# Performance work log

Measured on AMD Instinct MI355X. Metric: run time of the kernel, lower is better.

Reference implementation:

```python
import jax, jax.numpy as jnp
import numpy as np

EPSILON_BASE = 0.1
N_ITERS = 10


def setup_inputs() -> dict:
    key = jax.random.key(0)
    k1, k2 = jax.random.split(key)
    N, D = 8192, 512
    embeddings = jax.random.normal(k1, (N, D), dtype=jnp.float32)
    target_noise = jax.random.normal(k2, (N, D), dtype=jnp.float32)
    return {"embeddings": embeddings, "target_noise": target_noise}


def _l2_normalize(x, axis=1, eps=1e-12):
    # matches torch.nn.functional.normalize (divide by max(norm, eps))
    norm = jnp.sqrt(jnp.sum(x * x, axis=axis, keepdims=True))
    return x / jnp.maximum(norm, eps)


def _sinkhorn(x, y):
    n, d = x.shape
    # normalize_embeddings=True path
    x = _l2_normalize(x, axis=1)
    y = _l2_normalize(y, axis=1)
    epsilon = EPSILON_BASE * 2.0
    # squared euclidean cost: C[i,j] = ||x_i - y_j||^2  (cdist p=2, squared)
    sq_x = jnp.sum(x * x, axis=1, keepdims=True)          # (n,1)
    sq_y = jnp.sum(y * y, axis=1, keepdims=True)          # (n,1)
    C = jnp.maximum(sq_x + sq_y.T - 2.0 * (x @ y.T), 0.0)  # (n,n)
    log_K = -C / epsilon

    def body(carry, _):
        log_u, log_v = carry
        log_u = -jax.nn.logsumexp(log_K + log_v[None, :], axis=1)
        log_v = -jax.nn.logsumexp(log_K.T + log_u[None, :], axis=1)
        return (log_u, log_v), None

    init = (jnp.zeros(n, dtype=x.dtype), jnp.zeros(n, dtype=y.dtype))
    (log_u, log_v), _ = jax.lax.scan(body, init, None, length=N_ITERS)

    log_P = log_u[:, None] + log_K + log_v[None, :]
    P = jnp.clip(jnp.exp(log_P), 0.0, 1.0)
    distance = jnp.sum(P * C) / n

    # nan/inf fallback: 1 - mean cosine similarity (x, y already unit norm)
    fallback = 1.0 - jnp.mean(jnp.sum(x * y, axis=1))
    bad = jnp.isnan(distance) | jnp.isinf(distance)
    return jnp.where(bad, fallback, distance)


def reference(embeddings, target_noise):
    if embeddings.ndim == 3:
        embeddings = embeddings.reshape(-1, embeddings.shape[-1])
        target_noise = target_noise.reshape(-1, target_noise.shape[-1])
    return _sinkhorn(embeddings, target_noise)
```

## Files before the change

### kernel.cpp

```cpp
#include <hip/hip_runtime.h>
#include <hip/hip_bf16.h>
#include <hip/hip_fp16.h>
#include <stdint.h>

#define NROW 8192
#define DIM  512
#define LN2   0.6931471805599453f
#define TEN_LOG2E 14.426950408889634f

typedef __attribute__((ext_vector_type(8))) short short8;
typedef __attribute__((ext_vector_type(4))) float f32x4;
typedef __attribute__((ext_vector_type(2))) float f32x2;

__device__ __forceinline__ float block_sum256(float v) {
  #pragma unroll
  for (int off = 32; off > 0; off >>= 1) v += __shfl_down(v, off, 64);
  __shared__ float sb[4];
  const int w = threadIdx.x >> 6;
  if ((threadIdx.x & 63) == 0) sb[w] = v;
  __syncthreads();
  return sb[0] + sb[1] + sb[2] + sb[3];
}

__global__ __launch_bounds__(256) void init_kernel(float* __restrict__ colrcp,
                                                   float* __restrict__ diagacc,
                                                   float* __restrict__ distacc) {
  const int g = blockIdx.x * 256 + threadIdx.x;
  colrcp[g] = 1.0f;
  if (g == 0) { diagacc[0] = 0.f; distacc[0] = 0.f; }
}

__global__ __launch_bounds__(256) void normalize_kernel(
    const float* __restrict__ X, const float* __restrict__ Y,
    __hip_bfloat16* __restrict__ Xn, __hip_bfloat16* __restrict__ Yn,
    float* __restrict__ diagacc) {
  const int wave = threadIdx.x >> 6, lane = threadIdx.x & 63;
  float dsum = 0.f;
  #pragma unroll
  for (int rr = 0; rr < 4; rr++) {
    const int row = blockIdx.x * 16 + wave * 4 + rr;
    const float4* xr = (const float4*)(X + (size_t)row * DIM);
    const float4* yr = (const float4*)(Y + (size_t)row * DIM);
    float4 x0 = xr[lane], x1 = xr[lane + 64];
    float4 y0 = yr[lane], y1 = yr[lane + 64];
    float sx = x0.x*x0.x + x0.y*x0.y + x0.z*x0.z + x0.w*x0.w
             + x1.x*x1.x + x1.y*x1.y + x1.z*x1.z + x1.w*x1.w;
    float sy = y0.x*y0.x + y0.y*y0.y + y0.z*y0.z + y0.w*y0.w
             + y1.x*y1.x + y1.y*y1.y + y1.z*y1.z + y1.w*y1.w;
    float sxy = x0.x*y0.x + x0.y*y0.y + x0.z*y0.z + x0.w*y0.w
              + x1.x*y1.x + x1.y*y1.y + x1.z*y1.z + x1.w*y1.w;
    #pragma unroll
    for (int off = 1; off < 64; off <<= 1) {
      sx  += __shfl_xor(sx, off, 64);
      sy  += __shfl_xor(sy, off, 64);
      sxy += __shfl_xor(sxy, off, 64);
    }
    const float rx = 1.0f / fmaxf(sqrtf(sx), 1e-12f);
    const float ry = 1.0f / fmaxf(sqrtf(sy), 1e-12f);
    if (lane == 0) dsum += sxy * rx * ry;
    ushort4 px, py;
    { __hip_bfloat16 b;
      b = __float2bfloat16(x0.x*rx); px.x = *(unsigned short*)&b;
      b = __float2bfloat16(x0.y*rx); px.y = *(unsigned short*)&b;
      b = __float2bfloat16(x0.z*rx); px.z = *(unsigned short*)&b;
      b = __float2bfloat16(x0.w*rx); px.w = *(unsigned short*)&b;
      b = __float2bfloat16(y0.x*ry); py.x = *(unsigned short*)&b;
      b = __float2bfloat16(y0.y*ry); py.y = *(unsigned short*)&b;
      b = __float2bfloat16(y0.z*ry); py.z = *(unsigned short*)&b;
      b = __float2bfloat16(y0.w*ry); py.w = *(unsigned short*)&b;
    }
    ((ushort4*)(Xn + (size_t)row * DIM))[lane] = px;
    ((ushort4*)(Yn + (size_t)row * DIM))[lane] = py;
    { __hip_bfloat16 b;
      b = __float2bfloat16(x1.x*rx); px.x = *(unsigned short*)&b;
      b = __float2bfloat16(x1.y*rx); px.y = *(unsigned short*)&b;
      b = __float2bfloat16(x1.z*rx); px.z = *(unsigned short*)&b;
      b = __float2bfloat16(x1.w*rx); px.w = *(unsigned short*)&b;
      b = __float2bfloat16(y1.x*ry); py.x = *(unsigned short*)&b;
      b = __float2bfloat16(y1.y*ry); py.y = *(unsigned short*)&b;
      b = __float2bfloat16(y1.z*ry); py.z = *(unsigned short*)&b;
      b = __float2bfloat16(y1.w*ry); py.w = *(unsigned short*)&b;
    }
    ((ushort4*)(Xn + (size_t)row * DIM))[lane + 64] = px;
    ((ushort4*)(Yn + (size_t)row * DIM))[lane + 64] = py;
  }
  if (lane == 0) atomicAdd(diagacc, dsum);
}

__global__ __launch_bounds__(256) void gemm_kernel(
    const __hip_bfloat16* __restrict__ A, const __hip_bfloat16* __restrict__ B,
    uint8_t* __restrict__ K, uint8_t* __restrict__ KT) {
  __shared__ int4 smem4[1024];
  short* As = (short*)smem4;
  short* Bs = As + 128 * 32;
  const int m0 = blockIdx.y * 128;
  const int n0 = blockIdx.x * 128;
  const int t = threadIdx.x;
  const int wave = t >> 6, lane = t & 63;
  const int wm = (wave & 1) * 64, wn = (wave >> 1) * 64;
  const int fr = lane & 15;
  const int fq = lane >> 4;

  f32x4 acc[4][4];
  #pragma unroll
  for (int i = 0; i < 4; i++)
    #pragma unroll
    for (int j = 0; j < 4; j++) acc[i][j] = (f32x4)0.f;

  const int L0 = t, L1 = t + 256;
  const int ar0 = L0 >> 2, ac0 = L0 & 3;
  const int ar1 = L1 >> 2, ac1 = L1 & 3;
  const int4* Ag = (const int4*)A;
  const int4* Bg = (const int4*)B;

  for (int kt = 0; kt < 16; ++kt) {
    const int kb = kt * 4;
    int4 a0 = Ag[(size_t)(m0 + ar0) * 64 + kb + ac0];
    int4 a1 = Ag[(size_t)(m0 + ar1) * 64 + kb + ac1];
    int4 b0 = Bg[(size_t)(n0 + ar0) * 64 + kb + ac0];
    int4 b1 = Bg[(size_t)(n0 + ar1) * 64 + kb + ac1];
    __syncthreads();
    ((int4*)As)[L0] = a0;
    ((int4*)As)[L1] = a1;
    ((int4*)Bs)[L0] = b0;
    ((int4*)Bs)[L1] = b1;
    __syncthreads();
    short8 af[4], bfr[4];
    #pragma unroll
    for (int i = 0; i < 4; i++) {
      af[i]  = *(const short8*)&As[(wm + i * 16 + fr) * 32 + fq * 8];
      bfr[i] = *(const short8*)&Bs[(wn + i * 16 + fr) * 32 + fq * 8];
    }
    #pragma unroll
    for (int i = 0; i < 4; i++)
      #pragma unroll
      for (int j = 0; j < 4; j++)
        acc[i][j] = __builtin_amdgcn_mfma_f32_16x16x32_bf16(af[i], bfr[j], acc[i][j], 0, 0, 0);
  }
  __syncthreads();
  uint8_t* tile = (uint8_t*)smem4;
  #pragma unroll
  for (int i = 0; i < 4; i++) {
    #pragma unroll
    for (int j = 0; j < 4; j++) {
      const int R  = wm + i * 16 + fq * 4;
      const int Cc = wn + j * 16 + fr;
      float v0 = exp2f(fminf(acc[i][j][0], 1.0f) * TEN_LOG2E);
      float v1 = exp2f(fminf(acc[i][j][1], 1.0f) * TEN_LOG2E);
      float v2 = exp2f(fminf(acc[i][j][2], 1.0f) * TEN_LOG2E);
      float v3 = exp2f(fminf(acc[i][j][3], 1.0f) * TEN_LOG2E);
      int pk = 0;
      pk = __builtin_amdgcn_cvt_pk_fp8_f32(v0, v1, pk, false);
      pk = __builtin_amdgcn_cvt_pk_fp8_f32(v2, v3, pk, true);
      const int a = Cc * 128 + R;
      *(int*)(tile + (a ^ (((a >> 7) & 7) << 4))) = pk;
      uint8_t* kp = K + (size_t)(m0 + R) * NROW + n0 + Cc;
      kp[0]            = (uint8_t)(pk & 0xff);
      kp[NROW]         = (uint8_t)((pk >> 8) & 0xff);
      kp[2 * NROW]     = (uint8_t)((pk >> 16) & 0xff);
      kp[3 * NROW]     = (uint8_t)((pk >> 24) & 0xff);
    }
  }
  __syncthreads();
  {
    const int r = t >> 1, h = (t & 1) * 64;
    uint8_t* gp = KT + (size_t)(n0 + r) * NROW + m0 + h;
    #pragma unroll
    for (int q = 0; q < 4; q++) {
      const int a = r * 128 + h + q * 16;
      *(int4*)(gp + q * 16) = *(const int4*)(tile + (a ^ (((a >> 7) & 7) << 4)));
    }
  }
}

__global__ __launch_bounds__(256) void pass_kernel(
    const uint8_t* __restrict__ M, const float* __restrict__ w,
    float* __restrict__ out) {
  __shared__ float4 wl[2048];
  const int t = threadIdx.x;
  #pragma unroll
  for (int c = 0; c < 8; c++) {
    const int j = c * 256 + t;
    wl[j ^ ((j >> 3) & 3)] = ((const float4*)w)[j];
  }
  __syncthreads();
  const int wave = t >> 6, lane = t & 63;
  const int row = blockIdx.x * 4 + wave;
  const int xh = (lane >> 1) & 3;
  const int4* Mr = (const int4*)(M + (size_t)row * NROW);
  int4 k[8];
  #pragma unroll
  for (int c = 0; c < 8; c++) k[c] = Mr[c * 64 + lane];
  float acc0 = 0.f, acc1 = 0.f;
  #pragma unroll
  for (int c = 0; c < 8; c++) {
    const int b4 = (c * 64 + lane) * 4;
    const int* kd = (const int*)&k[c];
    #pragma unroll
    for (int q = 0; q < 4; q++) {
      float4 ww = wl[b4 + (q ^ xh)];
      f32x2 lo = __builtin_amdgcn_cvt_pk_f32_fp8(kd[q], false);
      f32x2 hi = __builtin_amdgcn_cvt_pk_f32_fp8(kd[q], true);
      acc0 += lo.x * ww.x + lo.y * ww.y;
      acc1 += hi.x * ww.z + hi.y * ww.w;
    }
  }
  float acc = acc0 + acc1;
  #pragma unroll
  for (int off = 32; off > 0; off >>= 1) acc += __shfl_down(acc, off, 64);
  if (lane == 0) out[row] = 1.0f / acc;
}

__global__ __launch_bounds__(256) void dist_kernel(
    const uint8_t* __restrict__ K, const float* __restrict__ v,
    const float* __restrict__ u, float* __restrict__ distacc) {
  __shared__ float4 wl[2048];
  const int t = threadIdx.x;
  #pragma unroll
  for (int c = 0; c < 8; c++) {
    const int j = c * 256 + t;
    wl[j ^ ((j >> 3) & 3)] = ((const float4*)v)[j];
  }
  __syncthreads();
  const int wave = t >> 6, lane = t & 63;
  const int row = blockIdx.x * 4 + wave;
  const int xh = (lane >> 1) & 3;
  const float ui = u[row];
  const int4* Kr = (const int4*)(K + (size_t)row * NROW);
  float acc = 0.f;
  #pragma unroll 2
  for (int c = 0; c < 8; c++) {
    int4 kq = Kr[c * 64 + lane];
    const int b4 = (c * 64 + lane) * 4;
    const int* kd = (const int*)&kq;
    #pragma unroll
    for (int q = 0; q < 4; q++) {
      float4 ww = wl[b4 + (q ^ xh)];
      f32x2 lo = __builtin_amdgcn_cvt_pk_f32_fp8(kd[q], false);
      f32x2 hi = __builtin_amdgcn_cvt_pk_f32_fp8(kd[q], true);
      float kv[4] = {lo.x, lo.y, hi.x, hi.y};
      float wv[4] = {ww.x, ww.y, ww.z, ww.w};
      #pragma unroll
      for (int e = 0; e < 4; e++) {
        float p = fminf(ui * kv[e] * wv[e], 1.f);
        float cterm = 2.f - 0.2f * LN2 * __log2f(fmaxf(kv[e], 1e-6f));
        acc += p * cterm;
      }
    }
  }
  float tot = block_sum256(acc);
  if (t == 0) atomicAdd(distacc, tot);
}

__global__ void final_kernel(const float* __restrict__ distacc,
                             const float* __restrict__ diagacc,
                             float* __restrict__ out) {
  if (threadIdx.x == 0 && blockIdx.x == 0) {
    float d = distacc[0] * (1.0f / (float)NROW);
    float fb = 1.0f - diagacc[0] * (1.0f / (float)NROW);
    float v = (isnan(d) || isinf(d)) ? fb : d;
    __hip_bfloat16 b = __float2bfloat16(v);
    unsigned short h = *(unsigned short*)&b;
    ((unsigned int*)out)[0] = ((unsigned int)h << 16) | (unsigned int)h;
  }
}

extern "C" void kernel_launch(void* const* d_in, const int* in_sizes, int n_in,
                              void* d_out, int out_size, void* d_ws, size_t ws_size,
                              hipStream_t stream) {
  (void)in_sizes; (void)n_in; (void)out_size; (void)ws_size;
  const float* X = (const float*)d_in[0];
  const float* Y = (const float*)d_in[1];
  float* out = (float*)d_out;

  char* ws = (char*)d_ws;
  size_t off = 0;
  uint8_t* K  = (uint8_t*)(ws + off); off += (size_t)NROW * NROW;
  uint8_t* KT = (uint8_t*)(ws + off); off += (size_t)NROW * NROW;
  __hip_bfloat16* Xn = (__hip_bfloat16*)(ws + off); off += (size_t)NROW * DIM * 2;
  __hip_bfloat16* Yn = (__hip_bfloat16*)(ws + off); off += (size_t)NROW * DIM * 2;
  float* rowrcp  = (float*)(ws + off); off += NROW * 4;
  float* colrcp  = (float*)(ws + off); off += NROW * 4;
  float* diagacc = (float*)(ws + off); off += 256;
  float* distacc = (float*)(ws + off); off += 256;

  init_kernel<<<32, 256, 0, stream>>>(colrcp, diagacc, distacc);
  normalize_kernel<<<512, 256, 0, stream>>>(X, Y, Xn, Yn, diagacc);
  gemm_kernel<<<dim3(64, 64), 256, 0, stream>>>(Xn, Yn, K, KT);
  for (int it = 0; it < 10; ++it) {
    pass_kernel<<<2048, 256, 0, stream>>>(K,  colrcp, rowrcp);
    pass_kernel<<<2048, 256, 0, stream>>>(KT, rowrcp, colrcp);
  }
  dist_kernel<<<2048, 256, 0, stream>>>(K, colrcp, rowrcp, distacc);
  final_kernel<<<1, 64, 0, stream>>>(distacc, diagacc, out);
}
```

Before: 489.2 us.

## Fuse final column pass with distance and process four rows per wave

Each wave in the pass kernel now handles four rows, double-buffering the next row's fp8 loads in registers. The weight vector is staged into LDS once per 16 rows instead of once per 4. The last column-scaling pass is merged into the distance kernel, which reads KT and computes v_j in registers before accumulating P*C, removing one full 64MB matrix sweep. The cost is fewer blocks (512) and higher register use, which may lower occupancy.

Result: no change. 493.2 us (+0.8%).

```diff
diff --git a/kernel.cpp b/kernel.cpp
--- a/kernel.cpp
+++ b/kernel.cpp
@@ -178,77 +178,115 @@
     float* __restrict__ out) {
   __shared__ float4 wl[2048];
   const int t = threadIdx.x;
+  const int wave = t >> 6, lane = t & 63;
+  const int xh = (lane >> 1) & 3;
+  const int row0 = blockIdx.x * 16 + wave * 4;
+  int4 ka[8], kb[8];
+  const int4* Mr0 = (const int4*)(M + (size_t)row0 * NROW);
+  #pragma unroll
+  for (int c = 0; c < 8; c++) ka[c] = Mr0[c * 64 + lane];
   #pragma unroll
   for (int c = 0; c < 8; c++) {
     const int j = c * 256 + t;
     wl[j ^ ((j >> 3) & 3)] = ((const float4*)w)[j];
   }
   __syncthreads();
-  const int wave = t >> 6, lane = t & 63;
-  const int row = blockIdx.x * 4 + wave;
-  const int xh = (lane >> 1) & 3;
-  const int4* Mr = (const int4*)(M + (size_t)row * NROW);
-  int4 k[8];
-  #pragma unroll
-  for (int c = 0; c < 8; c++) k[c] = Mr[c * 64 + lane];
-  float acc0 = 0.f, acc1 = 0.f;
-  #pragma unroll
-  for (int c = 0; c < 8; c++) {
-    const int b4 = (c * 64 + lane) * 4;
-    const int* kd = (const int*)&k[c];
-    #pragma unroll
-    for (int q = 0; q < 4; q++) {
-      float4 ww = wl[b4 + (q ^ xh)];
-      f32x2 lo = __builtin_amdgcn_cvt_pk_f32_fp8(kd[q], false);
-      f32x2 hi = __builtin_amdgcn_cvt_pk_f32_fp8(kd[q], true);
-      acc0 += lo.x * ww.x + lo.y * ww.y;
-      acc1 += hi.x * ww.z + hi.y * ww.w;
-    }
-  }
-  float acc = acc0 + acc1;
-  #pragma unroll
-  for (int off = 32; off > 0; off >>= 1) acc += __shfl_down(acc, off, 64);
-  if (lane == 0) out[row] = 1.0f / acc;
-}
-
-__global__ __launch_bounds__(256) void dist_kernel(
-    const uint8_t* __restrict__ K, const float* __restrict__ v,
-    const float* __restrict__ u, float* __restrict__ distacc) {
+  #pragma unroll
+  for (int r = 0; r < 4; r++) {
+    if (r < 3) {
+      const int4* Mn = (const int4*)(M + (size_t)(row0 + r + 1) * NROW);
+      #pragma unroll
+      for (int c = 0; c < 8; c++) { if (r & 1) ka[c] = Mn[c * 64 + lane]; else kb[c] = Mn[c * 64 + lane]; }
+    }
+    float acc0 = 0.f, acc1 = 0.f;
+    #pragma unroll
+    for (int c = 0; c < 8; c++) {
+      const int b4 = (c * 64 + lane) * 4;
+      const int4 kc = (r & 1) ? kb[c] : ka[c];
+      const int* kd = (const int*)&kc;
+      #pragma unroll
+      for (int q = 0; q < 4; q++) {
+        float4 ww = wl[b4 + (q ^ xh)];
+        f32x2 lo = __builtin_amdgcn_cvt_pk_f32_fp8(kd[q], false);
+        f32x2 hi = __builtin_amdgcn_cvt_pk_f32_fp8(kd[q], true);
+        acc0 += lo.x * ww.x + lo.y * ww.y;
+        acc1 += hi.x * ww.z + hi.y * ww.w;
+      }
+    }
+    float acc = acc0 + acc1;
+    #pragma unroll
+    for (int off = 32; off > 0; off >>= 1) acc += __shfl_down(acc, off, 64);
+    if (lane == 0) out[row0 + r] = 1.0f / acc;
+  }
+}
+
+__global__ __launch_bounds__(256) void pass_dist_kernel(
+    const uint8_t* __restrict__ KT, const float* __restrict__ u,
+    float* __restrict__ distacc) {
   __shared__ float4 wl[2048];
   const int t = threadIdx.x;
+  const int wave = t >> 6, lane = t & 63;
+  const int xh = (lane >> 1) & 3;
+  const int row0 = blockIdx.x * 16 + wave * 4;
+  int4 ka[8], kb[8];
+  const int4* Mr0 = (const int4*)(KT + (size_t)row0 * NROW);
+  #pragma unroll
+  for (int c = 0; c < 8; c++) ka[c] = Mr0[c * 64 + lane];
   #pragma unroll
   for (int c = 0; c < 8; c++) {
     const int j = c * 256 + t;
-    wl[j ^ ((j >> 3) & 3)] = ((const float4*)v)[j];
-  }
-  __syncthreads();
-  const int wave = t >> 6, lane = t & 63;
-  const int row = blockIdx.x * 4 + wave;
-  const int xh = (lane >> 1) & 3;
-  const float ui = u[row];
-  const int4* Kr = (const int4*)(K + (size_t)row * NROW);
-  float acc = 0.f;
-  #pragma unroll 2
-  for (int c = 0; c < 8; c++) {
-    int4 kq = Kr[c * 64 + lane];
-    const int b4 = (c * 64 + lane) * 4;
-    const int* kd = (const int*)&kq;
-    #pragma unroll
-    for (int q = 0; q < 4; q++) {
-      float4 ww = wl[b4 + (q ^ xh)];
-      f32x2 lo = __builtin_amdgcn_cvt_pk_f32_fp8(kd[q], false);
-      f32x2 hi = __builtin_amdgcn_cvt_pk_f32_fp8(kd[q], true);
-      float kv[4] = {lo.x, lo.y, hi.x, hi.y};
-      float wv[4] = {ww.x, ww.y, ww.z, ww.w};
-      #pragma unroll
-      for (int e = 0; e < 4; e++) {
-        float p = fminf(ui * kv[e] * wv[e], 1.f);
-        float cterm = 2.f - 0.2f * LN2 * __log2f(fmaxf(kv[e], 1e-6f));
-        acc += p * cterm;
+    wl[j ^ ((j >> 3) & 3)] = ((const float4*)u)[j];
+  }
+  __syncthreads();
+  float accd = 0.f;
+  #pragma unroll
+  for (int r = 0; r < 4; r++) {
+    if (r < 3) {
+      const int4* Mn = (const int4*)(KT + (size_t)(row0 + r + 1) * NROW);
+      #pragma unroll
+      for (int c = 0; c < 8; c++) { if (r & 1) ka[c] = Mn[c * 64 + lane]; else kb[c] = Mn[c * 64 + lane]; }
+    }
+    float acc0 = 0.f, acc1 = 0.f;
+    #pragma unroll
+    for (int c = 0; c < 8; c++) {
+      const int b4 = (c * 64 + lane) * 4;
+      const int4 kc = (r & 1) ? kb[c] : ka[c];
+      const int* kd = (const int*)&kc;
+      #pragma unroll
+      for (int q = 0; q < 4; q++) {
+        float4 ww = wl[b4 + (q ^ xh)];
+        f32x2 lo = __builtin_amdgcn_cvt_pk_f32_fp8(kd[q], false);
+        f32x2 hi = __builtin_amdgcn_cvt_pk_f32_fp8(kd[q], true);
+        acc0 += lo.x * ww.x + lo.y * ww.y;
+        acc1 += hi.x * ww.z + hi.y * ww.w;
       }
     }
-  }
-  float tot = block_sum256(acc);
+    float s = acc0 + acc1;
+    #pragma unroll
+    for (int off = 1; off < 64; off <<= 1) s += __shfl_xor(s, off, 64);
+    const float vj = 1.0f / s;
+    #pragma unroll
+    for (int c = 0; c < 8; c++) {
+      const int b4 = (c * 64 + lane) * 4;
+      const int4 kc = (r & 1) ? kb[c] : ka[c];
+      const int* kd = (const int*)&kc;
+      #pragma unroll
+      for (int q = 0; q < 4; q++) {
+        float4 ww = wl[b4 + (q ^ xh)];
+        f32x2 lo = __builtin_amdgcn_cvt_pk_f32_fp8(kd[q], false);
+        f32x2 hi = __builtin_amdgcn_cvt_pk_f32_fp8(kd[q], true);
+        float kv[4] = {lo.x, lo.y, hi.x, hi.y};
+        float uv[4] = {ww.x, ww.y, ww.z, ww.w};
+        #pragma unroll
+        for (int e = 0; e < 4; e++) {
+          float p = fminf(uv[e] * kv[e] * vj, 1.f);
+          float cterm = 2.f - 0.2f * LN2 * __log2f(fmaxf(kv[e], 1e-6f));
+          accd += p * cterm;
+        }
+      }
+    }
+  }
+  float tot = block_sum256(accd);
   if (t == 0) atomicAdd(distacc, tot);
 }
 
@@ -288,9 +326,10 @@
   normalize_kernel<<<512, 256, 0, stream>>>(X, Y, Xn, Yn, diagacc);
   gemm_kernel<<<dim3(64, 64), 256, 0, stream>>>(Xn, Yn, K, KT);
   for (int it = 0; it < 10; ++it) {
-    pass_kernel<<<2048, 256, 0, stream>>>(K,  colrcp, rowrcp);
-    pass_kernel<<<2048, 256, 0, stream>>>(KT, rowrcp, colrcp);
-  }
-  dist_kernel<<<2048, 256, 0, stream>>>(K, colrcp, rowrcp, distacc);
+    pass_kernel<<<512, 256, 0, stream>>>(K,  colrcp, rowrcp);
+    if (it < 9)
+      pass_kernel<<<512, 256, 0, stream>>>(KT, rowrcp, colrcp);
+  }
+  pass_dist_kernel<<<512, 256, 0, stream>>>(KT, rowrcp, distacc);
   final_kernel<<<1, 64, 0, stream>>>(distacc, diagacc, out);
 }
```
